# Performance work log

Measured on AMD Instinct MI355X. Metric: run time of the kernel, lower is better.

## Reference

```python
import jax, jax.numpy as jnp
import numpy as np

D_IN = 1024
D_OUT = 1024
CTX_LEN = 2048
BATCH = 4
SEQ = 2048


def setup_inputs() -> dict:
    key = jax.random.key(0)
    kx, kq, kk, kv = jax.random.split(key, 4)
    x = jax.random.normal(kx, (BATCH, SEQ, D_IN), dtype=jnp.float32)
    s = 1.0 / np.sqrt(D_IN)
    # torch nn.Linear weight is (d_out, d_in); store transposed for x @ W
    W_q = jax.random.uniform(kq, (D_IN, D_OUT), dtype=jnp.float32, minval=-s, maxval=s)
    W_k = jax.random.uniform(kk, (D_IN, D_OUT), dtype=jnp.float32, minval=-s, maxval=s)
    W_v = jax.random.uniform(kv, (D_IN, D_OUT), dtype=jnp.float32, minval=-s, maxval=s)
    return {"x": x, "W_q": W_q, "W_k": W_k, "W_v": W_v}


def reference(x, W_q, W_k, W_v):
    b, n, _ = x.shape
    d_out = W_q.shape[1]
    q = x @ W_q            # [b, n, d_out]
    k = x @ W_k
    v = x @ W_v
    scores = jnp.einsum('bqd,bkd->bqk', q, k)  # [b, n, n]
    causal = jnp.triu(jnp.ones((n, n), dtype=bool), k=1)
    scores = jnp.where(causal, -jnp.inf, scores)
    attn = jax.nn.softmax(scores / jnp.sqrt(jnp.float32(d_out)), axis=-1)
    # dropout p=0.0 -> identity
    return jnp.einsum('bqk,bkd->bqd', attn, v)
```

## Files before the change

### kernel.cpp

```cpp
#include <hip/hip_runtime.h>
#include <hip/hip_bf16.h>

#define BATCH 4
#define SEQ   2048
#define DIN   1024
#define DOUT  1024
#define N3    3072
#define MTOT  (BATCH*SEQ)

typedef __hip_bfloat16 bf16;
typedef __attribute__((ext_vector_type(8))) short bf16x8;
typedef __attribute__((ext_vector_type(4))) float f32x4;

#define MFMA(a,b,c) __builtin_amdgcn_mfma_f32_16x16x32_bf16(a,b,c,0,0,0)

union pack4 { bf16 h[4]; uint2 u2; };
union pack8 { bf16 h[8]; bf16x8 v; };

__device__ __forceinline__ void gl16(const bf16* g, bf16* l)
{
    __builtin_amdgcn_global_load_lds(
        (const __attribute__((address_space(1))) void*)g,
        (__attribute__((address_space(3))) void*)l, 16, 0, 0);
}


__global__ __launch_bounds__(256)
void k_prep(const float* __restrict__ x, const float* __restrict__ Wq,
            const float* __restrict__ Wk, const float* __restrict__ Wv,
            bf16* __restrict__ xb, bf16* __restrict__ Wt)
{
    __shared__ bf16 t[64][68];
    const int bid = blockIdx.x;
    if (bid < 8192) {
        long i = ((long)bid * 256 + threadIdx.x) * 4;
        float4 v = *(const float4*)(x + i);
        pack4 o;
        o.h[0] = __float2bfloat16(v.x);
        o.h[1] = __float2bfloat16(v.y);
        o.h[2] = __float2bfloat16(v.z);
        o.h[3] = __float2bfloat16(v.w);
        *(uint2*)(xb + i) = o.u2;
        return;
    }
    const int idx = bid - 8192;
    const int mat = idx >> 8;
    const int rem = idx & 255;
    const int k0 = (rem >> 4) * 64, n0 = (rem & 15) * 64;
    const float* W = (mat == 0) ? Wq : ((mat == 1) ? Wk : Wv);
#pragma unroll
    for (int p = 0; p < 4; ++p) {
        int kr = p * 16 + (threadIdx.x >> 4);
        int c4 = (threadIdx.x & 15) * 4;
        float4 v = *(const float4*)&W[(long)(k0 + kr) * DOUT + n0 + c4];
        t[c4 + 0][kr] = __float2bfloat16(v.x);
        t[c4 + 1][kr] = __float2bfloat16(v.y);
        t[c4 + 2][kr] = __float2bfloat16(v.z);
        t[c4 + 3][kr] = __float2bfloat16(v.w);
    }
    __syncthreads();
    bf16* O = Wt + (long)mat * DIN * DOUT;
#pragma unroll
    for (int i = 0; i < 2; ++i) {
        int l = threadIdx.x + i * 256;
        int n = l >> 3, c8 = (l & 7) * 8;
        pack8 o;
#pragma unroll
        for (int j = 0; j < 8; ++j) o.h[j] = t[n][c8 + j];
        *(bf16x8*)&O[(long)(n0 + n) * DIN + k0 + c8] = o.v;
    }
}


#define BAR() do { __builtin_amdgcn_sched_barrier(0); \
                   __builtin_amdgcn_s_barrier();      \
                   __builtin_amdgcn_sched_barrier(0); } while (0)

__global__ __launch_bounds__(512, 2)
void k_gemm_qkv(const bf16* __restrict__ xb, const bf16* __restrict__ Wt,
                bf16* __restrict__ QK, bf16* __restrict__ Vt)
{
    __shared__ __align__(16) bf16 smem[49152];
    bf16* sA = smem;
    bf16* sB = smem + 16384;

    const int tid = threadIdx.x;
    const int m0 = blockIdx.y * 128;
    const int n0 = blockIdx.x * 256;

    const bf16* Abase = xb + (long)m0 * DIN;
    const bf16* Bbase = Wt + (long)n0 * DIN;

    const int srow = tid >> 3;
    const int scol = ((tid & 7) ^ (srow & 7)) * 8;

    const int lane = tid & 63, wave = tid >> 6;
    const int wr = wave >> 2, wc = wave & 3;
    const int r = lane & 15, qd = lane >> 4;
    const int aRow  = (wr * 64 + r) * 64;
    const int bHalf = wc >> 1;
    const int bRow  = ((wc & 1) * 64 + r) * 64;
    const int slot0 = ( qd      ^ (r & 7)) * 8;
    const int slot1 = ((4 + qd) ^ (r & 7)) * 8;

    auto stageA = [&](int kt, int pass) {
        const bf16* src = Abase + (long)(srow + pass * 64) * DIN + kt * 64 + scol;
        gl16(src, &sA[(kt & 1) * 8192 + pass * 4096 + tid * 8]);
    };
    auto stageB = [&](int kt, int half, int pass) {
        const bf16* src = Bbase + (long)(half * 128 + srow + pass * 64) * DIN + kt * 64 + scol;
        gl16(src, &sB[(kt & 1) * 16384 + half * 8192 + pass * 4096 + tid * 8]);
    };

    f32x4 acc[4][4] = {};

    stageB(0, 0, 0); stageB(0, 0, 1); stageB(0, 1, 0); stageB(0, 1, 1);
    stageA(0, 0);    stageA(0, 1);
    stageB(1, 0, 0); stageB(1, 0, 1); stageB(1, 1, 0);
    asm volatile("s_waitcnt vmcnt(3)" ::: "memory");
    BAR();

#pragma unroll 2
    for (int kt = 0; kt < 16; ++kt) {
        const int c = kt & 1;
        const bf16* A = sA + c * 8192;
        const bf16* B = sB + c * 16384 + bHalf * 8192;

        bf16x8 bv[4][2], af[2][2];
#pragma unroll
        for (int ni = 0; ni < 4; ++ni) {
            bv[ni][0] = *(const bf16x8*)&B[bRow + ni * 1024 + slot0];
            bv[ni][1] = *(const bf16x8*)&B[bRow + ni * 1024 + slot1];
        }
#pragma unroll
        for (int mi = 0; mi < 2; ++mi) {
            af[mi][0] = *(const bf16x8*)&A[aRow + mi * 1024 + slot0];
            af[mi][1] = *(const bf16x8*)&A[aRow + mi * 1024 + slot1];
        }
        if (kt + 1 < 16) { stageB(kt + 1, 1, 1); stageA(kt + 1, 0); stageA(kt + 1, 1); }
        BAR();
        asm volatile("s_waitcnt lgkmcnt(0)" ::: "memory");
        __builtin_amdgcn_s_setprio(1);
#pragma unroll
        for (int mi = 0; mi < 2; ++mi)
#pragma unroll
            for (int ni = 0; ni < 4; ++ni) {
                acc[mi][ni] = MFMA(af[mi][0], bv[ni][0], acc[mi][ni]);
                acc[mi][ni] = MFMA(af[mi][1], bv[ni][1], acc[mi][ni]);
            }
        __builtin_amdgcn_s_setprio(0);
        BAR();

        bf16x8 ag[2][2];
#pragma unroll
        for (int mi = 0; mi < 2; ++mi) {
            ag[mi][0] = *(const bf16x8*)&A[aRow + (mi + 2) * 1024 + slot0];
            ag[mi][1] = *(const bf16x8*)&A[aRow + (mi + 2) * 1024 + slot1];
        }
        if (kt + 2 < 16) { stageB(kt + 2, 0, 0); stageB(kt + 2, 0, 1); stageB(kt + 2, 1, 0); }
        BAR();
        asm volatile("s_waitcnt lgkmcnt(0)" ::: "memory");
        __builtin_amdgcn_s_setprio(1);
#pragma unroll
        for (int mi = 0; mi < 2; ++mi)
#pragma unroll
            for (int ni = 0; ni < 4; ++ni) {
                acc[mi + 2][ni] = MFMA(ag[mi][0], bv[ni][0], acc[mi + 2][ni]);
                acc[mi + 2][ni] = MFMA(ag[mi][1], bv[ni][1], acc[mi + 2][ni]);
            }
        __builtin_amdgcn_s_setprio(0);
        if (kt < 14)       { asm volatile("s_waitcnt vmcnt(3)" ::: "memory"); }
        else if (kt == 14) { asm volatile("s_waitcnt vmcnt(0)" ::: "memory"); }
        BAR();
    }

    const int bx = blockIdx.x;
    if (bx < 8) {
#pragma unroll
        for (int mi = 0; mi < 4; ++mi)
#pragma unroll
            for (int ni = 0; ni < 4; ++ni)
#pragma unroll
                for (int j = 0; j < 4; ++j) {
                    int row = m0 + wr * 64 + mi * 16 + qd * 4 + j;
                    int col = n0 + wc * 64 + ni * 16 + r;
                    QK[(long)row * 2048 + col] = __float2bfloat16(acc[mi][ni][j]);
                }
    } else {
        const int ld = 136;
        bf16* T = smem;
#pragma unroll
        for (int mi = 0; mi < 4; ++mi)
#pragma unroll
            for (int ni = 0; ni < 4; ++ni) {
                pack4 p;
#pragma unroll
                for (int j = 0; j < 4; ++j) p.h[j] = __float2bfloat16(acc[mi][ni][j]);
                int d_l = wc * 64 + ni * 16 + r;
                int s_l = wr * 64 + mi * 16 + qd * 4;
                *(uint2*)&T[d_l * ld + s_l] = p.u2;
            }
        __syncthreads();
        const int n0v = n0 - 2048;
        const int bb = m0 >> 11;
        const int s0 = m0 & 2047;
        bf16* Ob = Vt + (long)bb * DOUT * SEQ + s0;
#pragma unroll
        for (int p = 0; p < 8; ++p) {
            int l = tid + p * 512;
            int d = l >> 4, s8 = (l & 15) * 8;
            bf16x8 vv = *(const bf16x8*)&T[d * ld + s8];
            *(bf16x8*)&Ob[(long)(n0v + d) * SEQ + s8] = vv;
        }
    }
}


__device__ __forceinline__ void gemm_core(
    const bf16* __restrict__ Ab, long lda,
    const bf16* __restrict__ Bb, long ldb,
    int nk, bf16* __restrict__ As, bf16* __restrict__ Bs,
    f32x4 acc[4][4])
{
    const int tid  = threadIdx.x;
    const int lane = tid & 63;
    const int wave = tid >> 6;
    const int wm = (wave >> 1) * 64;
    const int wn = (wave & 1) * 64;
    const int r  = lane & 15;
    const int qd = lane >> 4;

    const int row0 = tid >> 3;
    const int c    = (tid & 7) ^ (row0 & 7);
    const long aoff = (long)row0 * lda + c * 8;
    const long boff = (long)row0 * ldb + c * 8;
    const long astep = 32 * lda, bstep = 32 * ldb;
    bf16* dA = &As[tid * 8];
    bf16* dB = &Bs[tid * 8];

    for (int kk = 0; kk < nk; ++kk) {
        const bf16* A = Ab + kk * 64 + aoff;
        const bf16* B = Bb + kk * 64 + boff;
#pragma unroll
        for (int i = 0; i < 4; ++i) {
            gl16(A + i * astep, dA + i * 2048);
            gl16(B + i * bstep, dB + i * 2048);
        }
        __syncthreads();
#pragma unroll
        for (int ks = 0; ks < 2; ++ks) {
            const int slot = ((ks * 4 + qd) ^ (r & 7)) * 8;
            bf16x8 af[4], bv[4];
#pragma unroll
            for (int mi = 0; mi < 4; ++mi)
                af[mi] = *(const bf16x8*)&As[(wm + mi * 16 + r) * 64 + slot];
#pragma unroll
            for (int ni = 0; ni < 4; ++ni)
                bv[ni] = *(const bf16x8*)&Bs[(wn + ni * 16 + r) * 64 + slot];
#pragma unroll
            for (int mi = 0; mi < 4; ++mi)
#pragma unroll
                for (int ni = 0; ni < 4; ++ni)
                    acc[mi][ni] = MFMA(af[mi], bv[ni], acc[mi][ni]);
        }
        __syncthreads();
    }
}


__global__ __launch_bounds__(256, 3)
void k_gemm_scores(const bf16* __restrict__ QK, bf16* __restrict__ P,
                   float* __restrict__ rowSum)
{
    const int b = blockIdx.z, qt = blockIdx.y, kt = blockIdx.x;
    if (kt > qt) return;
    __shared__ __align__(16) bf16 As[128 * 64];
    __shared__ __align__(16) bf16 Bs[128 * 64];
    const bf16* A  = QK + (long)b * SEQ * 2048;
    const bf16* Bt = A + 1024;
    f32x4 acc[4][4] = {};
    gemm_core(A + (long)qt * 128 * 2048, 2048, Bt + (long)kt * 128 * 2048, 2048,
              DIN / 64, As, Bs, acc);

    bf16* Pb = P + (long)b * SEQ * SEQ;
    float* RS = rowSum + b * SEQ;
    const int lane = threadIdx.x & 63, wave = threadIdx.x >> 6;
    const int wm = (wave >> 1) * 64, wn = (wave & 1) * 64;
    const int r = lane & 15, qd = lane >> 4;

    float rp[4][4];
#pragma unroll
    for (int mi = 0; mi < 4; ++mi)
#pragma unroll
        for (int j = 0; j < 4; ++j) rp[mi][j] = 0.f;

#pragma unroll
    for (int mi = 0; mi < 4; ++mi)
#pragma unroll
        for (int ni = 0; ni < 4; ++ni)
#pragma unroll
            for (int j = 0; j < 4; ++j) {
                int row = qt * 128 + wm + mi * 16 + qd * 4 + j;
                int col = kt * 128 + wn + ni * 16 + r;
                float e = (col > row) ? 0.f : __expf(acc[mi][ni][j] * 0.03125f);
                rp[mi][j] += e;
                Pb[(long)row * SEQ + col] = __float2bfloat16(e);
            }
#pragma unroll
    for (int d = 1; d < 16; d <<= 1)
#pragma unroll
        for (int mi = 0; mi < 4; ++mi)
#pragma unroll
            for (int j = 0; j < 4; ++j)
                rp[mi][j] += __shfl_xor(rp[mi][j], d, 64);
    if (r == 0) {
#pragma unroll
        for (int mi = 0; mi < 4; ++mi)
#pragma unroll
            for (int j = 0; j < 4; ++j) {
                int row = qt * 128 + wm + mi * 16 + qd * 4 + j;
                atomicAdd(&RS[row], rp[mi][j]);
            }
    }
}


__global__ __launch_bounds__(256, 3)
void k_gemm_pv(const bf16* __restrict__ P, const bf16* __restrict__ Vt,
               const float* __restrict__ rowSum, float* __restrict__ O)
{
    const int b = blockIdx.z, nt = blockIdx.x;
    const int qt = (SEQ / 128 - 1) - blockIdx.y;
    __shared__ __align__(16) bf16 As[128 * 64];
    __shared__ __align__(16) bf16 Bs[128 * 64];
    const bf16* A  = P + (long)b * SEQ * SEQ + (long)qt * 128 * SEQ;
    const bf16* Bt = Vt + (long)b * DOUT * SEQ;
    const int nk = (qt + 1) * 2;
    f32x4 acc[4][4] = {};
    gemm_core(A, SEQ, Bt + (long)nt * 128 * SEQ, SEQ, nk, As, Bs, acc);

    float* Ob = O + (long)b * SEQ * DOUT;
    const float* RS = rowSum + b * SEQ;
    const int lane = threadIdx.x & 63, wave = threadIdx.x >> 6;
    const int wm = (wave >> 1) * 64, wn = (wave & 1) * 64;
    const int r = lane & 15, qd = lane >> 4;
#pragma unroll
    for (int mi = 0; mi < 4; ++mi)
#pragma unroll
        for (int j = 0; j < 4; ++j) {
            int row = qt * 128 + wm + mi * 16 + qd * 4 + j;
            float inv = 1.0f / RS[row];
#pragma unroll
            for (int ni = 0; ni < 4; ++ni) {
                int col = nt * 128 + wn + ni * 16 + r;
                Ob[(long)row * DOUT + col] = acc[mi][ni][j] * inv;
            }
        }
}


extern "C" void kernel_launch(void* const* d_in, const int* in_sizes, int n_in,
                              void* d_out, int out_size, void* d_ws, size_t ws_size,
                              hipStream_t stream)
{
    const float* x  = (const float*)d_in[0];
    const float* Wq = (const float*)d_in[1];
    const float* Wk = (const float*)d_in[2];
    const float* Wv = (const float*)d_in[3];
    float* out = (float*)d_out;

    char* ws = (char*)d_ws;
    bf16*  xb = (bf16*)(ws);
    bf16*  Wt = (bf16*)(ws + 16777216);
    bf16*  QK = (bf16*)(ws + 23068672);
    bf16*  Vt = (bf16*)(ws + 56623104);
    bf16*  P  = (bf16*)(ws + 73400320);
    float* RS = (float*)(ws + 106954752);

    hipMemsetAsync(RS, 0, BATCH * SEQ * sizeof(float), stream);
    k_prep<<<dim3(8192 + 768), 256, 0, stream>>>(x, Wq, Wk, Wv, xb, Wt);
    k_gemm_qkv<<<dim3(N3 / 256, MTOT / 128), 512, 0, stream>>>(xb, Wt, QK, Vt);
    k_gemm_scores<<<dim3(SEQ / 128, SEQ / 128, BATCH), 256, 0, stream>>>(QK, P, RS);
    k_gemm_pv<<<dim3(DOUT / 128, SEQ / 128, BATCH), 256, 0, stream>>>(P, Vt, RS, out);
}
```

Baseline: 222.5 us.

## Restructure QKV GEMM main loop with one barrier per k-tile and XCD swizzle

Replaces the multi-barrier ping-pong schedule in the QKV projection GEMM with a simpler loop. Each iteration issues all global-to-LDS loads for the next k-tile, then interleaves LDS fragment reads with four MFMA groups, using lgkmcnt waits instead of barriers, and ends with one full vmcnt(0) wait and barrier. It also remaps workgroup IDs so that consecutive tiles are spread across XCDs (8-way modulo swizzle), aiming at better L2 locality. The cost is that the global prefetch is now only one tile deep and must fully complete before every barrier, which may expose memory latency. The partial lgkmcnt counts also rely on the compiler emitting the LDS reads in source order.

```diff
diff --git a/kernel.cpp b/kernel.cpp
--- a/kernel.cpp
+++ b/kernel.cpp
@@ -72,9 +72,8 @@
 }
 
 
-#define BAR() do { __builtin_amdgcn_sched_barrier(0); \
-                   __builtin_amdgcn_s_barrier();      \
-                   __builtin_amdgcn_sched_barrier(0); } while (0)
+#define WAITLG(n) do { asm volatile("s_waitcnt lgkmcnt(" #n ")" ::: "memory"); \
+                       __builtin_amdgcn_sched_barrier(0); } while (0)
 
 __global__ __launch_bounds__(512, 2)
 void k_gemm_qkv(const bf16* __restrict__ xb, const bf16* __restrict__ Wt,
@@ -85,8 +84,12 @@
     bf16* sB = smem + 16384;
 
     const int tid = threadIdx.x;
-    const int m0 = blockIdx.y * 128;
-    const int n0 = blockIdx.x * 256;
+
+    const int wg  = blockIdx.y * 12 + blockIdx.x;
+    const int swz = (wg & 7) * 96 + (wg >> 3);
+    const int bx  = swz % 12, by = swz / 12;
+    const int m0 = by * 128;
+    const int n0 = bx * 256;
 
     const bf16* Abase = xb + (long)m0 * DIN;
     const bf16* Bbase = Wt + (long)n0 * DIN;
@@ -116,9 +119,10 @@
 
     stageB(0, 0, 0); stageB(0, 0, 1); stageB(0, 1, 0); stageB(0, 1, 1);
     stageA(0, 0);    stageA(0, 1);
-    stageB(1, 0, 0); stageB(1, 0, 1); stageB(1, 1, 0);
-    asm volatile("s_waitcnt vmcnt(3)" ::: "memory");
-    BAR();
+    asm volatile("s_waitcnt vmcnt(0)" ::: "memory");
+    __builtin_amdgcn_sched_barrier(0);
+    __builtin_amdgcn_s_barrier();
+    __builtin_amdgcn_sched_barrier(0);
 
 #pragma unroll 2
     for (int kt = 0; kt < 16; ++kt) {
@@ -126,55 +130,70 @@
         const bf16* A = sA + c * 8192;
         const bf16* B = sB + c * 16384 + bHalf * 8192;
 
-        bf16x8 bv[4][2], af[2][2];
+        if (kt + 1 < 16) {
+            stageB(kt + 1, 0, 0); stageB(kt + 1, 0, 1);
+            stageB(kt + 1, 1, 0); stageB(kt + 1, 1, 1);
+            stageA(kt + 1, 0);    stageA(kt + 1, 1);
+        }
+
+        bf16x8 a0[2], a1[2], a2[2], a3[2], b0[4], b1[4];
+
+        a0[0] = *(const bf16x8*)&A[aRow + 0 * 1024 + slot0];
+        a0[1] = *(const bf16x8*)&A[aRow + 1 * 1024 + slot0];
+#pragma unroll
+        for (int ni = 0; ni < 4; ++ni)
+            b0[ni] = *(const bf16x8*)&B[bRow + ni * 1024 + slot0];
+        a1[0] = *(const bf16x8*)&A[aRow + 2 * 1024 + slot0];
+        a1[1] = *(const bf16x8*)&A[aRow + 3 * 1024 + slot0];
+        WAITLG(2);
+        __builtin_amdgcn_s_setprio(1);
 #pragma unroll
         for (int ni = 0; ni < 4; ++ni) {
-            bv[ni][0] = *(const bf16x8*)&B[bRow + ni * 1024 + slot0];
-            bv[ni][1] = *(const bf16x8*)&B[bRow + ni * 1024 + slot1];
-        }
-#pragma unroll
-        for (int mi = 0; mi < 2; ++mi) {
-            af[mi][0] = *(const bf16x8*)&A[aRow + mi * 1024 + slot0];
-            af[mi][1] = *(const bf16x8*)&A[aRow + mi * 1024 + slot1];
-        }
-        if (kt + 1 < 16) { stageB(kt + 1, 1, 1); stageA(kt + 1, 0); stageA(kt + 1, 1); }
-        BAR();
-        asm volatile("s_waitcnt lgkmcnt(0)" ::: "memory");
+            acc[0][ni] = MFMA(a0[0], b0[ni], acc[0][ni]);
+            acc[1][ni] = MFMA(a0[1], b0[ni], acc[1][ni]);
+        }
+        __builtin_amdgcn_s_setprio(0);
+
+        a2[0] = *(const bf16x8*)&A[aRow + 0 * 1024 + slot1];
+        a2[1] = *(const bf16x8*)&A[aRow + 1 * 1024 + slot1];
+#pragma unroll
+        for (int ni = 0; ni < 4; ++ni)
+            b1[ni] = *(const bf16x8*)&B[bRow + ni * 1024 + slot1];
+        WAITLG(6);
         __builtin_amdgcn_s_setprio(1);
 #pragma unroll
-        for (int mi = 0; mi < 2; ++mi)
-#pragma unroll
-            for (int ni = 0; ni < 4; ++ni) {
-                acc[mi][ni] = MFMA(af[mi][0], bv[ni][0], acc[mi][ni]);
-                acc[mi][ni] = MFMA(af[mi][1], bv[ni][1], acc[mi][ni]);
-            }
+        for (int ni = 0; ni < 4; ++ni) {
+            acc[2][ni] = MFMA(a1[0], b0[ni], acc[2][ni]);
+            acc[3][ni] = MFMA(a1[1], b0[ni], acc[3][ni]);
+        }
         __builtin_amdgcn_s_setprio(0);
-        BAR();
-
-        bf16x8 ag[2][2];
-#pragma unroll
-        for (int mi = 0; mi < 2; ++mi) {
-            ag[mi][0] = *(const bf16x8*)&A[aRow + (mi + 2) * 1024 + slot0];
-            ag[mi][1] = *(const bf16x8*)&A[aRow + (mi + 2) * 1024 + slot1];
-        }
-        if (kt + 2 < 16) { stageB(kt + 2, 0, 0); stageB(kt + 2, 0, 1); stageB(kt + 2, 1, 0); }
-        BAR();
-        asm volatile("s_waitcnt lgkmcnt(0)" ::: "memory");
+
+        a3[0] = *(const bf16x8*)&A[aRow + 2 * 1024 + slot1];
+        a3[1] = *(const bf16x8*)&A[aRow + 3 * 1024 + slot1];
+        WAITLG(2);
         __builtin_amdgcn_s_setprio(1);
 #pragma unroll
-        for (int mi = 0; mi < 2; ++mi)
-#pragma unroll
-            for (int ni = 0; ni < 4; ++ni) {
-                acc[mi + 2][ni] = MFMA(ag[mi][0], bv[ni][0], acc[mi + 2][ni]);
-                acc[mi + 2][ni] = MFMA(ag[mi][1], bv[ni][1], acc[mi + 2][ni]);
-            }
+        for (int ni = 0; ni < 4; ++ni) {
+            acc[0][ni] = MFMA(a2[0], b1[ni], acc[0][ni]);
+            acc[1][ni] = MFMA(a2[1], b1[ni], acc[1][ni]);
+        }
         __builtin_amdgcn_s_setprio(0);
-        if (kt < 14)       { asm volatile("s_waitcnt vmcnt(3)" ::: "memory"); }
-        else if (kt == 14) { asm volatile("s_waitcnt vmcnt(0)" ::: "memory"); }
-        BAR();
-    }
-
-    const int bx = blockIdx.x;
+
+        WAITLG(0);
+        __builtin_amdgcn_s_setprio(1);
+#pragma unroll
+        for (int ni = 0; ni < 4; ++ni) {
+            acc[2][ni] = MFMA(a3[0], b1[ni], acc[2][ni]);
+            acc[3][ni] = MFMA(a3[1], b1[ni], acc[3][ni]);
+        }
+        __builtin_amdgcn_s_setprio(0);
+
+        asm volatile("s_waitcnt vmcnt(0)" ::: "memory");
+        __builtin_amdgcn_sched_barrier(0);
+        __builtin_amdgcn_s_barrier();
+        __builtin_amdgcn_sched_barrier(0);
+    }
+
     if (bx < 8) {
 #pragma unroll
         for (int mi = 0; mi < 4; ++mi)
```

Measured after the change: 221.7 us. No clear change (-0.3%).
